# Performance work log

Hardware: AMD Instinct MI355X
Metric: run time of the kernel (lower is better)

Reference implementation:

```python
import jax, jax.numpy as jnp
import numpy as np
from math import sqrt

BASE = 10000.0  # rope_theta
NUM_HEADS = 16


def _quant(x):
    # per-row (last-dim) symmetric int8 fake-quant, matching ActivationQuantSTE.forward
    scale = 127.0 / jnp.maximum(jnp.max(jnp.abs(x), axis=-1, keepdims=True), 1e-5)
    return jnp.clip(jnp.round(x * scale), -128.0, 127.0) / scale


@jax.custom_vjp
def act_quant(x):
    return _quant(x)

def _aq_fwd(x):
    return _quant(x), None

def _aq_bwd(_, g):
    return (g,)  # straight-through estimator

act_quant.defvjp(_aq_fwd, _aq_bwd)


def complex_linear(xr, xi, Wr, Wi):
    # ComplexLinearBase: quantize activations, then
    #   y_real = q_real @ Wr^T + q_imag @ Wi^T
    #   y_imag = q_real @ Wi^T - q_imag @ Wr^T
    qr = act_quant(xr)
    qi = act_quant(xi)
    yr = qr @ Wr.T + qi @ Wi.T
    yi = qr @ Wi.T - qi @ Wr.T
    return yr, yi


def setup_inputs() -> dict:
    T, H = 2048, 2048
    key = jax.random.key(0)
    ks = jax.random.split(key, 10)
    w = lambda k: jax.random.normal(k, (H, H), jnp.float32) * 0.02
    return {
        "hidden_real": jax.random.normal(ks[0], (T, H), jnp.float32),
        "hidden_imag": jax.random.normal(ks[1], (T, H), jnp.float32),
        "positions": jnp.arange(T, dtype=jnp.int32),
        "Wq_r": w(ks[2]), "Wq_i": w(ks[3]),
        "Wk_r": w(ks[4]), "Wk_i": w(ks[5]),
        "Wv_r": w(ks[6]), "Wv_i": w(ks[7]),
        "Wo_r": w(ks[8]), "Wo_i": w(ks[9]),
    }


def reference(hidden_real, hidden_imag, positions, Wq_r, Wq_i, Wk_r, Wk_i, Wv_r, Wv_i, Wo_r, Wo_i):
    T, H = hidden_real.shape
    NH = NUM_HEADS
    D = H // NH  # head_dim

    # complex QKV projections with int8 activation fake-quant
    qr, qi = complex_linear(hidden_real, hidden_imag, Wq_r, Wq_i)
    kr, ki = complex_linear(hidden_real, hidden_imag, Wk_r, Wk_i)
    vr, vi = complex_linear(hidden_real, hidden_imag, Wv_r, Wv_i)

    # Complex RoPE: interleaving (real, imag) then GPT-J-style rotation with
    # head_size = rotary_dim = 2*D is equivalent to rotating (real, imag) pairs:
    #   out_real = real*cos - imag*sin ; out_imag = imag*cos + real*sin
    # inv_freq = base^-(arange(0, 2D, 2)/(2D)) = base^-(arange(D)/D), len D.
    inv_freq = 1.0 / (BASE ** (jnp.arange(D, dtype=jnp.float32) / D))
    freqs = positions.astype(jnp.float32)[:, None] * inv_freq[None, :]  # [T, D]
    # cache is stored in bf16 in the original module
    cos = jnp.cos(freqs).astype(jnp.bfloat16).astype(jnp.float32)[:, None, :]  # [T,1,D]
    sin = jnp.sin(freqs).astype(jnp.bfloat16).astype(jnp.float32)[:, None, :]

    def rope(xr_, xi_):
        r = xr_.reshape(T, NH, D)
        i = xi_.reshape(T, NH, D)
        return r * cos - i * sin, i * cos + r * sin

    qr3, qi3 = rope(qr, qi)
    kr3, ki3 = rope(kr, ki)
    vr3 = vr.reshape(T, NH, D)
    vi3 = vi.reshape(T, NH, D)

    # causal attention; scores = Re(q . conj(k)) / sqrt(2*D)  (complex dim is 2*D)
    scale = 1.0 / sqrt(2 * D)
    scores = (jnp.einsum('thd,shd->hts', qr3, kr3)
              + jnp.einsum('thd,shd->hts', qi3, ki3)) * scale  # [NH, T, T]
    causal = jnp.tril(jnp.ones((T, T), dtype=bool))
    scores = jnp.where(causal[None], scores, -1e9)
    p = jax.nn.softmax(scores, axis=-1)

    out_r = jnp.einsum('hts,shd->thd', p, vr3).reshape(T, H)
    out_i = jnp.einsum('hts,shd->thd', p, vi3).reshape(T, H)

    # complex output projection (with activation fake-quant)
    return complex_linear(out_r, out_i, Wo_r, Wo_i)
```

## Files before the change

### kernel.cpp

```cpp
#include <hip/hip_runtime.h>


typedef float v4f __attribute__((ext_vector_type(4)));
typedef _Float16 v8h __attribute__((ext_vector_type(8)));
typedef _Float16 v4h __attribute__((ext_vector_type(4)));

typedef const __attribute__((address_space(1))) void glob_void;
typedef __attribute__((address_space(3))) void lds_void;

__device__ __forceinline__ void gload16(const _Float16* gp, _Float16* lp) {
  __builtin_amdgcn_global_load_lds((glob_void*)gp, (lds_void*)lp, 16, 0, 0);
}

__device__ __forceinline__ float bf16_rt(float f) {
  union { float f; unsigned u; } a; a.f = f;
  unsigned r = (a.u + 0x7fffu + ((a.u >> 16) & 1u)) & 0xffff0000u;
  union { unsigned u; float f; } b; b.u = r;
  return b.f;
}

#define EPI_QKV 0
#define EPI_OUT 1

__global__ __launch_bounds__(512, 2) void gemm_qkv256(
    const _Float16* __restrict__ A, const _Float16* __restrict__ B,
    _Float16* __restrict__ Yq, _Float16* __restrict__ vt)
{
  const int p = blockIdx.x;
  const int xcd = p & 7, s = p >> 3;
  const int mt = s & 7, ntl = s >> 3;
  const int nt = xcd * 8 + ntl;
  const int m0 = mt << 8;
  const int n0 = nt * 192;

  __shared__ __align__(16) _Float16 lds[57344];

  const int tid = threadIdx.x, lane = tid & 63, wave = tid >> 6;
  const int quad = lane >> 4, l15 = lane & 15;
  const int wm = wave >> 2, wn = wave & 3;

  const int rr = tid >> 2;
  const int lc8 = (((tid & 3) ^ ((tid >> 3) & 3)) << 3);
  const _Float16* gA = A + (long long)(m0 + rr) * 4096 + lc8;
  const _Float16* gBj[3];
#pragma unroll
  for (int j = 0; j < 3; ++j) {
    const int ks = (j == 2) || (j == 1 && tid >= 256);
    const int r = j * 128 + (tid >> 2) - ks * 192;
    gBj[j] = B + (long long)(n0 + r) * 4096 + ks * 32 + lc8;
  }

  const int co = ((quad ^ ((l15 >> 1) & 3)) << 3);
  const int aBase = (wm * 128 + l15) * 32 + co;
  const int bBase = (wn * 48 + l15) * 32 + co;

  v4f acc[8][3] = {};

  auto stage = [&](int b, int k0) {
    _Float16* dst = lds + b * 28672 + tid * 8;
#pragma unroll
    for (int j = 0; j < 4; ++j)
      gload16(gA + k0 + (j & 1) * (128 * 4096) + ((j >> 1) << 5), dst + j * 4096);
#pragma unroll
    for (int j = 0; j < 3; ++j)
      gload16(gBj[j] + k0, dst + 16384 + j * 4096);
  };

  stage(0, 0);

  for (int t = 0; t < 64; ++t) {
    const int buf = t & 1;
    __builtin_amdgcn_s_barrier();
    if (t < 63) {
      stage(buf ^ 1, (t + 1) << 6);
      asm volatile("s_waitcnt vmcnt(7)" ::: "memory");
    } else {
      asm volatile("s_waitcnt vmcnt(0)" ::: "memory");
    }
    __builtin_amdgcn_s_barrier();

    const _Float16* As = lds + buf * 28672;
    const _Float16* Bs = As + 16384;
    v8h bf[3][2];
#pragma unroll
    for (int nf = 0; nf < 3; ++nf)
#pragma unroll
      for (int ks = 0; ks < 2; ++ks)
        bf[nf][ks] = *(const v8h*)&Bs[bBase + ks * 6144 + nf * 512];
#pragma unroll
    for (int mh = 0; mh < 2; ++mh) {
      v8h af[4][2];
#pragma unroll
      for (int i = 0; i < 4; ++i)
#pragma unroll
        for (int ks = 0; ks < 2; ++ks)
          af[i][ks] = *(const v8h*)&As[aBase + ks * 8192 + (mh * 4 + i) * 512];
      __builtin_amdgcn_s_setprio(1);
#pragma unroll
      for (int i = 0; i < 4; ++i)
#pragma unroll
        for (int nf = 0; nf < 3; ++nf)
#pragma unroll
          for (int ks = 0; ks < 2; ++ks)
            acc[mh * 4 + i][nf] = __builtin_amdgcn_mfma_f32_16x16x32_f16(
                af[i][ks], bf[nf][ks], acc[mh * 4 + i][nf], 0, 0, 0);
      __builtin_amdgcn_s_setprio(0);
    }
  }

#pragma unroll
  for (int mf = 0; mf < 8; ++mf) {
#pragma unroll
    for (int nf = 0; nf < 3; ++nf) {
      const int col = n0 + wn * 48 + nf * 16 + l15;
      const int row0 = m0 + wm * 128 + mf * 16 + quad * 4;
      if (col >= 8192) {
        const int c = col - 8192;
        const int hh = (c & 2047) >> 7;
        const int dcol = (c < 2048) ? (c & 127) : (128 + (c & 127));
        v4h pk;
#pragma unroll
        for (int r = 0; r < 4; ++r) pk[r] = (_Float16)acc[mf][nf][r];
        *(v4h*)(vt + ((long long)(hh * 256 + dcol)) * 2048 + row0) = pk;
      } else {
#pragma unroll
        for (int r = 0; r < 4; ++r)
          Yq[(long long)(row0 + r) * 8192 + col] = (_Float16)acc[mf][nf][r];
      }
    }
  }
}

template<int EPI>
__global__ __launch_bounds__(256) void gemm_nt(
    const _Float16* __restrict__ A, const _Float16* __restrict__ B,
    void* __restrict__ Cv, int K, int lda, int ldb, int ldc,
    _Float16* __restrict__ vtout)
{
  const int m0 = blockIdx.x * 128, n0 = blockIdx.y * 128;

  __shared__ __align__(16) _Float16 As[128 * 32];
  __shared__ __align__(16) _Float16 Bs[128 * 32];

  const int tid = threadIdx.x, lane = tid & 63, wave = tid >> 6;
  const int off0 = tid * 8, off1 = 2048 + tid * 8;
  const int r0 = off0 >> 5, r1 = off1 >> 5;
  const int c0 = ((((off0 >> 3) & 3) ^ ((r0 >> 1) & 3)) << 3);
  const int c1 = ((((off1 >> 3) & 3) ^ ((r1 >> 1) & 3)) << 3);
  const _Float16* ga0 = A + (long long)(m0 + r0) * lda + c0;
  const _Float16* ga1 = A + (long long)(m0 + r1) * lda + c1;
  const _Float16* gb0 = B + (long long)(n0 + r0) * ldb + c0;
  const _Float16* gb1 = B + (long long)(n0 + r1) * ldb + c1;

  const int mr = (wave >> 1) * 64 + (lane & 15);
  const int nr = (wave & 1) * 64 + (lane & 15);
  const int kq = lane >> 4;

  v4f acc[4][4] = {};

  for (int k0 = 0; k0 < K; k0 += 32) {
    gload16(ga0 + k0, As + off0);
    gload16(ga1 + k0, As + off1);
    gload16(gb0 + k0, Bs + off0);
    gload16(gb1 + k0, Bs + off1);
    __syncthreads();
    v8h a[4], b[4];
#pragma unroll
    for (int i = 0; i < 4; ++i) {
      const int r = mr + i * 16;
      a[i] = *(const v8h*)&As[r * 32 + ((kq ^ ((r >> 1) & 3)) << 3)];
    }
#pragma unroll
    for (int j = 0; j < 4; ++j) {
      const int r = nr + j * 16;
      b[j] = *(const v8h*)&Bs[r * 32 + ((kq ^ ((r >> 1) & 3)) << 3)];
    }
#pragma unroll
    for (int i = 0; i < 4; ++i)
#pragma unroll
      for (int j = 0; j < 4; ++j)
        acc[i][j] = __builtin_amdgcn_mfma_f32_16x16x32_f16(a[i], b[j], acc[i][j], 0, 0, 0);
    __syncthreads();
  }

  const int cr = (wave >> 1) * 64 + (lane >> 4) * 4;
  const int cc = (wave & 1) * 64 + (lane & 15);
#pragma unroll
  for (int i = 0; i < 4; ++i)
#pragma unroll
    for (int j = 0; j < 4; ++j) {
      const int col = n0 + cc + j * 16;
      if (EPI == EPI_QKV && col >= 8192) {
        const int c = col - 8192;
        const int hh = (c & 2047) >> 7;
        const int dcol = (c < 2048) ? (c & 127) : (128 + (c & 127));
        const int row0 = m0 + cr + i * 16;
        v4h pk;
#pragma unroll
        for (int r = 0; r < 4; ++r) pk[r] = (_Float16)acc[i][j][r];
        *(v4h*)(vtout + ((long long)(hh * 256 + dcol)) * 2048 + row0) = pk;
      } else {
#pragma unroll
        for (int r = 0; r < 4; ++r) {
          const int row = m0 + cr + i * 16 + r;
          const float v = acc[i][j][r];
          if (EPI == EPI_QKV) {
            ((_Float16*)Cv)[(long long)row * ldc + col] = (_Float16)v;
          } else {
            float* O = (float*)Cv;
            if (col < 2048) O[(long long)row * 2048 + col] = v;
            else O[2048ll * 2048 + (long long)row * 2048 + (col - 2048)] = v;
          }
        }
      }
    }
}

__global__ __launch_bounds__(256) void quant_rows(
    const float* __restrict__ s0, const float* __restrict__ s1,
    _Float16* __restrict__ dst)
{
  const int t = blockIdx.x, y = blockIdx.y;
  const float* src = (y ? s1 : s0) + (long long)t * 2048;
  const int tid = threadIdx.x, lane = tid & 63, wave = tid >> 6;
  __shared__ float rbuf[4];
  const v4f a = *(const v4f*)(src + tid * 4);
  const v4f b = *(const v4f*)(src + 1024 + tid * 4);
  float m = 0.f;
#pragma unroll
  for (int k = 0; k < 4; ++k)
    m = fmaxf(m, fmaxf(fabsf(a[k]), fabsf(b[k])));
  for (int o = 1; o < 64; o <<= 1) m = fmaxf(m, __shfl_xor(m, o, 64));
  if (lane == 0) rbuf[wave] = m;
  __syncthreads();
  m = fmaxf(fmaxf(rbuf[0], rbuf[1]), fmaxf(rbuf[2], rbuf[3]));
  const float scale = 127.f / fmaxf(m, 1e-5f);
  const float inv = 1.f / scale;
  _Float16* d = dst + (long long)t * 4096 + (long long)y * 2048 + tid * 4;
  v4h qa, qb;
#pragma unroll
  for (int k = 0; k < 4; ++k) {
    qa[k] = (_Float16)(fminf(fmaxf(rintf(a[k] * scale), -128.f), 127.f) * inv);
    qb[k] = (_Float16)(fminf(fmaxf(rintf(b[k] * scale), -128.f), 127.f) * inv);
  }
  *(v4h*)d = qa;
  *(v4h*)(d + 1024) = qb;
}

__global__ __launch_bounds__(256) void wprep(
    const float* __restrict__ Wq_r, const float* __restrict__ Wq_i,
    const float* __restrict__ Wk_r, const float* __restrict__ Wk_i,
    const float* __restrict__ Wv_r, const float* __restrict__ Wv_i,
    const float* __restrict__ Wo_r, const float* __restrict__ Wo_i,
    _Float16* __restrict__ Bqkv, _Float16* __restrict__ Bo)
{
  const float* Ws[8] = {Wq_r, Wq_i, Wk_r, Wk_i, Wv_r, Wv_i, Wo_r, Wo_i};
  const int i = blockIdx.x * 256 + threadIdx.x;
  const int w = i >> 18;
  const int rem = i & 262143;
  const int j = rem >> 7;
  const int cb = (rem & 127) * 16;
  const float* src = Ws[w] + (long long)j * 2048 + cb;
  _Float16* Bp = (w < 6) ? (Bqkv + (long long)(w >> 1) * 4096 * 4096) : Bo;
  const int isI = w & 1;
  _Float16* d1 = Bp + (long long)j * 4096 + (isI ? 2048 + cb : cb);
  _Float16* d2 = Bp + (long long)(2048 + j) * 4096 + (isI ? cb : 2048 + cb);
  const float sg2 = isI ? 1.f : -1.f;
#pragma unroll
  for (int q = 0; q < 4; ++q) {
    const v4f v = *(const v4f*)(src + q * 4);
    v4h o1, o2;
#pragma unroll
    for (int k = 0; k < 4; ++k) {
      o1[k] = (_Float16)v[k];
      o2[k] = (_Float16)(v[k] * sg2);
    }
    *(v4h*)(d1 + q * 4) = o1;
    *(v4h*)(d2 + q * 4) = o2;
  }
}

__global__ __launch_bounds__(256) void trig_kernel(
    const int* __restrict__ pos, float* __restrict__ cs)
{
  const int t = blockIdx.x * 2 + (threadIdx.x >> 7);
  const int d = threadIdx.x & 127;
  const float invf = (float)pow(10000.0, -(double)d / 128.0);
  const float fr = (float)pos[t] * invf;
  const double fd = (double)fr;
  cs[((long long)t * 128 + d) * 2]     = bf16_rt((float)cos(fd));
  cs[((long long)t * 128 + d) * 2 + 1] = bf16_rt((float)sin(fd));
}

__global__ __launch_bounds__(256) void rope_kernel(
    const _Float16* __restrict__ Yq, const float* __restrict__ cs,
    _Float16* __restrict__ qc, _Float16* __restrict__ kc)
{
  const int idx = blockIdx.x * 256 + threadIdx.x;
  const int d0 = (idx & 15) * 8;
  const int h  = (idx >> 4) & 15;
  const int t  = idx >> 8;
  const _Float16* y = Yq + (long long)t * 8192 + h * 128 + d0;
  const v8h qr8 = *(const v8h*)(y);
  const v8h qi8 = *(const v8h*)(y + 2048);
  const v8h kr8 = *(const v8h*)(y + 4096);
  const v8h ki8 = *(const v8h*)(y + 6144);
  const float* cp = cs + ((long long)t * 128 + d0) * 2;
  v8h qro, qio, kro, kio;
#pragma unroll
  for (int u = 0; u < 8; ++u) {
    const float c = cp[u * 2], s = cp[u * 2 + 1];
    const float qr = (float)qr8[u], qi = (float)qi8[u];
    const float kr = (float)kr8[u], ki = (float)ki8[u];
    qro[u] = (_Float16)(qr * c - qi * s);
    qio[u] = (_Float16)(qi * c + qr * s);
    kro[u] = (_Float16)(kr * c - ki * s);
    kio[u] = (_Float16)(ki * c + kr * s);
  }
  _Float16* qo = qc + ((long long)h * 2048 + t) * 256 + d0;
  _Float16* ko = kc + ((long long)h * 2048 + t) * 256 + d0;
  *(v8h*)qo = qro; *(v8h*)(qo + 128) = qio;
  *(v8h*)ko = kro; *(v8h*)(ko + 128) = kio;
}

__global__ __launch_bounds__(256, 2) void flash_attn(
    const _Float16* __restrict__ qc, const _Float16* __restrict__ kc,
    const _Float16* __restrict__ vt, float* __restrict__ attn)
{
  __shared__ __align__(16) _Float16 Ps[64 * 72];
  __shared__ float pmax[2][64];
  __shared__ float psum[2][64];

  const int h  = blockIdx.y;
  const int qt = ((h >> 3) & 1) ? (31 - (int)blockIdx.x) : (int)blockIdx.x;
  const int q0 = qt * 64;
  const int tid = threadIdx.x, lane = tid & 63, wave = tid >> 6;
  const int mi = wave >> 1, ni = wave & 1;
  const int quad = lane >> 4, l15 = lane & 15;

  const _Float16* qh = qc + (long long)h * 2048 * 256;
  const _Float16* kh = kc + (long long)h * 2048 * 256;
  const _Float16* vh = vt + (long long)h * 256 * 2048;

  const _Float16 scl = (_Float16)0.09016844f;
  v8h qf[2][8];
#pragma unroll
  for (int mt = 0; mt < 2; ++mt) {
    const int t = q0 + mi * 32 + mt * 16 + l15;
#pragma unroll
    for (int ks = 0; ks < 8; ++ks) {
      v8h q = *(const v8h*)(qh + (long long)t * 256 + ks * 32 + quad * 8);
#pragma unroll
      for (int u = 0; u < 8; ++u) q[u] *= scl;
      qf[mt][ks] = q;
    }
  }

  float mrow[2][4], lrow[2][4];
  v4f acc_o[2][8];
#pragma unroll
  for (int mt = 0; mt < 2; ++mt)
#pragma unroll
    for (int r = 0; r < 4; ++r) { mrow[mt][r] = -1e30f; lrow[mt][r] = 0.f; }
#pragma unroll
  for (int mt = 0; mt < 2; ++mt)
#pragma unroll
    for (int nt = 0; nt < 8; ++nt) acc_o[mt][nt] = (v4f){0.f, 0.f, 0.f, 0.f};

  for (int st = 0; st <= qt; ++st) {
    const int s0 = st * 64;

    v4f sa[2][2] = {};
#pragma unroll
    for (int ks = 0; ks < 8; ++ks) {
      v8h bk[2];
#pragma unroll
      for (int jn = 0; jn < 2; ++jn)
        bk[jn] = *(const v8h*)(kh + (long long)(s0 + ni * 32 + jn * 16 + l15) * 256
                               + ks * 32 + quad * 8);
#pragma unroll
      for (int mt = 0; mt < 2; ++mt)
#pragma unroll
        for (int jn = 0; jn < 2; ++jn)
          sa[mt][jn] = __builtin_amdgcn_mfma_f32_16x16x32_f16(qf[mt][ks], bk[jn], sa[mt][jn], 0, 0, 0);
    }

    const bool diag = (st == qt);
    float pm[2][4];
#pragma unroll
    for (int mt = 0; mt < 2; ++mt)
#pragma unroll
      for (int r = 0; r < 4; ++r) pm[mt][r] = -1e30f;
#pragma unroll
    for (int mt = 0; mt < 2; ++mt)
#pragma unroll
      for (int jn = 0; jn < 2; ++jn)
#pragma unroll
        for (int r = 0; r < 4; ++r) {
          float v = sa[mt][jn][r];
          if (diag) {
            const int rl = mi * 32 + mt * 16 + quad * 4 + r;
            const int cl = ni * 32 + jn * 16 + l15;
            if (cl > rl) v = -1e30f;
          }
          sa[mt][jn][r] = v;
          pm[mt][r] = fmaxf(pm[mt][r], v);
        }
#pragma unroll
    for (int o = 1; o < 16; o <<= 1)
#pragma unroll
      for (int mt = 0; mt < 2; ++mt)
#pragma unroll
        for (int r = 0; r < 4; ++r)
          pm[mt][r] = fmaxf(pm[mt][r], __shfl_xor(pm[mt][r], o, 64));
    if (l15 == 0) {
#pragma unroll
      for (int mt = 0; mt < 2; ++mt)
#pragma unroll
        for (int r = 0; r < 4; ++r)
          pmax[ni][mi * 32 + mt * 16 + quad * 4 + r] = pm[mt][r];
    }
    __syncthreads();

    float al[2][4], ps[2][4];
#pragma unroll
    for (int mt = 0; mt < 2; ++mt)
#pragma unroll
      for (int r = 0; r < 4; ++r) {
        const int row = mi * 32 + mt * 16 + quad * 4 + r;
        const float mn = fmaxf(mrow[mt][r], fmaxf(pmax[0][row], pmax[1][row]));
        al[mt][r] = __builtin_amdgcn_exp2f(mrow[mt][r] - mn);
        mrow[mt][r] = mn;
        ps[mt][r] = 0.f;
      }
#pragma unroll
    for (int mt = 0; mt < 2; ++mt)
#pragma unroll
      for (int jn = 0; jn < 2; ++jn)
#pragma unroll
        for (int r = 0; r < 4; ++r) {
          const float e = __builtin_amdgcn_exp2f(sa[mt][jn][r] - mrow[mt][r]);
          ps[mt][r] += e;
          Ps[(mi * 32 + mt * 16 + quad * 4 + r) * 72 + ni * 32 + jn * 16 + l15] = (_Float16)e;
        }
#pragma unroll
    for (int o = 1; o < 16; o <<= 1)
#pragma unroll
      for (int mt = 0; mt < 2; ++mt)
#pragma unroll
        for (int r = 0; r < 4; ++r)
          ps[mt][r] += __shfl_xor(ps[mt][r], o, 64);
    if (l15 == 0) {
#pragma unroll
      for (int mt = 0; mt < 2; ++mt)
#pragma unroll
        for (int r = 0; r < 4; ++r)
          psum[ni][mi * 32 + mt * 16 + quad * 4 + r] = ps[mt][r];
    }
    __syncthreads();

#pragma unroll
    for (int mt = 0; mt < 2; ++mt)
#pragma unroll
      for (int r = 0; r < 4; ++r) {
        const int row = mi * 32 + mt * 16 + quad * 4 + r;
        lrow[mt][r] = lrow[mt][r] * al[mt][r] + psum[0][row] + psum[1][row];
      }
#pragma unroll
    for (int mt = 0; mt < 2; ++mt)
#pragma unroll
      for (int nt = 0; nt < 8; ++nt)
#pragma unroll
        for (int r = 0; r < 4; ++r)
          acc_o[mt][nt][r] *= al[mt][r];

#pragma unroll
    for (int kc2 = 0; kc2 < 2; ++kc2) {
      v8h pa[2];
#pragma unroll
      for (int mt = 0; mt < 2; ++mt) {
        const int row = mi * 32 + mt * 16 + l15;
        pa[mt] = *(const v8h*)(Ps + row * 72 + kc2 * 32 + quad * 8);
      }
#pragma unroll
      for (int nt = 0; nt < 8; ++nt) {
        const v8h vb = *(const v8h*)(vh + (long long)(ni * 128 + nt * 16 + l15) * 2048
                                     + s0 + kc2 * 32 + quad * 8);
#pragma unroll
        for (int mt = 0; mt < 2; ++mt)
          acc_o[mt][nt] = __builtin_amdgcn_mfma_f32_16x16x32_f16(pa[mt], vb, acc_o[mt][nt], 0, 0, 0);
      }
    }
  }

#pragma unroll
  for (int mt = 0; mt < 2; ++mt) {
    float inv[4];
#pragma unroll
    for (int r = 0; r < 4; ++r) inv[r] = 1.f / lrow[mt][r];
#pragma unroll
    for (int nt = 0; nt < 8; ++nt) {
      const int d = ni * 128 + nt * 16 + l15;
      float* dst = attn + ((d < 128) ? 0ll : (2048ll * 2048)) + (h * 128 + (d & 127));
#pragma unroll
      for (int r = 0; r < 4; ++r) {
        const int t = q0 + mi * 32 + mt * 16 + quad * 4 + r;
        dst[(long long)t * 2048] = acc_o[mt][nt][r] * inv[r];
      }
    }
  }
}

extern "C" void kernel_launch(void* const* d_in, const int* in_sizes, int n_in,
                              void* d_out, int out_size, void* d_ws, size_t ws_size,
                              hipStream_t stream) {
  const float* hr   = (const float*)d_in[0];
  const float* hi   = (const float*)d_in[1];
  const int*   pos  = (const int*)d_in[2];
  const float* Wq_r = (const float*)d_in[3];
  const float* Wq_i = (const float*)d_in[4];
  const float* Wk_r = (const float*)d_in[5];
  const float* Wk_i = (const float*)d_in[6];
  const float* Wv_r = (const float*)d_in[7];
  const float* Wv_i = (const float*)d_in[8];
  const float* Wo_r = (const float*)d_in[9];
  const float* Wo_i = (const float*)d_in[10];

  char* ws = (char*)d_ws;
  _Float16* Bqkv = (_Float16*)(ws);
  float*    attn = (float*)   (ws);
  float*    cs   = (float*)   (ws + (32ll  << 20));
  _Float16* Bo   = (_Float16*)(ws + (96ll  << 20));
  _Float16* Ac   = (_Float16*)(ws + (128ll << 20));
  _Float16* Yq   = (_Float16*)(ws + (144ll << 20));
  _Float16* qc   = (_Float16*)(ws + (176ll << 20));
  _Float16* kc   = (_Float16*)(ws + (192ll << 20));
  _Float16* vt   = (_Float16*)(ws + (208ll << 20));

  quant_rows<<<dim3(2048, 2), 256, 0, stream>>>(hr, hi, Ac);
  wprep<<<8192, 256, 0, stream>>>(Wq_r, Wq_i, Wk_r, Wk_i, Wv_r, Wv_i, Wo_r, Wo_i, Bqkv, Bo);
  gemm_qkv256<<<512, 512, 0, stream>>>(Ac, Bqkv, Yq, vt);
  trig_kernel<<<1024, 256, 0, stream>>>(pos, cs);
  rope_kernel<<<2048, 256, 0, stream>>>(Yq, cs, qc, kc);
  flash_attn<<<dim3(32, 16), 256, 0, stream>>>(qc, kc, vt, attn);
  quant_rows<<<dim3(2048, 2), 256, 0, stream>>>(attn, attn + 2048ll * 2048, Ac);
  gemm_nt<EPI_OUT><<<dim3(16, 32), 256, 0, stream>>>(
      Ac, Bo, d_out, 4096, 4096, 4096, 0, nullptr);
}
```

Before: 735.0 us.

## Interleave QKV GEMM global-to-LDS staging with MFMA phases in ping-pong schedule

Restructures the QKV projection GEMM main loop into four sub-phases per k-tile. Each phase issues a slice of the next tile's global-to-LDS loads alongside LDS fragment reads and a 12-MFMA cluster, with explicit barriers and vmcnt waits, instead of staging the whole tile up front. This spreads memory traffic across the compute and reduces fragment register pressure. It adds several workgroup barriers per iteration, and the split vmcnt bookkeeping is fragile.

```diff
diff --git a/kernel.cpp b/kernel.cpp
--- a/kernel.cpp
+++ b/kernel.cpp
@@ -21,6 +21,10 @@
 
 #define EPI_QKV 0
 #define EPI_OUT 1
+
+#define SBAR()  __builtin_amdgcn_sched_barrier(0)
+#define WBAR()  __builtin_amdgcn_s_barrier()
+#define LGKM0() asm volatile("s_waitcnt lgkmcnt(0)" ::: "memory")
 
 __global__ __launch_bounds__(512, 2) void gemm_qkv256(
     const _Float16* __restrict__ A, const _Float16* __restrict__ B,
@@ -56,56 +60,96 @@
 
   v4f acc[8][3] = {};
 
-  auto stage = [&](int b, int k0) {
-    _Float16* dst = lds + b * 28672 + tid * 8;
-#pragma unroll
-    for (int j = 0; j < 4; ++j)
-      gload16(gA + k0 + (j & 1) * (128 * 4096) + ((j >> 1) << 5), dst + j * 4096);
-#pragma unroll
-    for (int j = 0; j < 3; ++j)
-      gload16(gBj[j] + k0, dst + 16384 + j * 4096);
-  };
-
-  stage(0, 0);
+  {
+    _Float16* sd = lds + tid * 8;
+    gload16(gA, sd);
+    gload16(gA + 524288, sd + 4096);
+    gload16(gBj[0], sd + 16384);
+    gload16(gBj[1], sd + 20480);
+    gload16(gA + 32, sd + 8192);
+    gload16(gA + 524288 + 32, sd + 12288);
+    gload16(gBj[2], sd + 24576);
+  }
+  asm volatile("s_waitcnt vmcnt(3)" ::: "memory");
+  WBAR();
 
   for (int t = 0; t < 64; ++t) {
-    const int buf = t & 1;
-    __builtin_amdgcn_s_barrier();
-    if (t < 63) {
-      stage(buf ^ 1, (t + 1) << 6);
-      asm volatile("s_waitcnt vmcnt(7)" ::: "memory");
-    } else {
-      asm volatile("s_waitcnt vmcnt(0)" ::: "memory");
-    }
-    __builtin_amdgcn_s_barrier();
-
-    const _Float16* As = lds + buf * 28672;
+    const _Float16* As = lds + (t & 1) * 28672;
     const _Float16* Bs = As + 16384;
-    v8h bf[3][2];
-#pragma unroll
-    for (int nf = 0; nf < 3; ++nf)
-#pragma unroll
-      for (int ks = 0; ks < 2; ++ks)
-        bf[nf][ks] = *(const v8h*)&Bs[bBase + ks * 6144 + nf * 512];
-#pragma unroll
-    for (int mh = 0; mh < 2; ++mh) {
-      v8h af[4][2];
-#pragma unroll
-      for (int i = 0; i < 4; ++i)
-#pragma unroll
-        for (int ks = 0; ks < 2; ++ks)
-          af[i][ks] = *(const v8h*)&As[aBase + ks * 8192 + (mh * 4 + i) * 512];
-      __builtin_amdgcn_s_setprio(1);
-#pragma unroll
-      for (int i = 0; i < 4; ++i)
-#pragma unroll
-        for (int nf = 0; nf < 3; ++nf)
-#pragma unroll
-          for (int ks = 0; ks < 2; ++ks)
-            acc[mh * 4 + i][nf] = __builtin_amdgcn_mfma_f32_16x16x32_f16(
-                af[i][ks], bf[nf][ks], acc[mh * 4 + i][nf], 0, 0, 0);
-      __builtin_amdgcn_s_setprio(0);
-    }
+    _Float16* sd = lds + ((t & 1) ^ 1) * 28672 + tid * 8;
+    const int k1 = (t + 1) << 6;
+    const bool stg = (t < 63);
+
+    v8h bf[3], af[4];
+
+    af[0] = *(const v8h*)&As[aBase];
+    af[1] = *(const v8h*)&As[aBase + 512];
+    af[2] = *(const v8h*)&As[aBase + 1024];
+    af[3] = *(const v8h*)&As[aBase + 1536];
+    bf[0] = *(const v8h*)&Bs[bBase];
+    bf[1] = *(const v8h*)&Bs[bBase + 512];
+    bf[2] = *(const v8h*)&Bs[bBase + 1024];
+    if (stg) { gload16(gA + k1, sd); gload16(gA + k1 + 524288, sd + 4096); }
+    SBAR(); WBAR(); LGKM0(); SBAR();
+    __builtin_amdgcn_s_setprio(1);
+#pragma unroll
+    for (int i = 0; i < 4; ++i)
+#pragma unroll
+      for (int nf = 0; nf < 3; ++nf)
+        acc[i][nf] = __builtin_amdgcn_mfma_f32_16x16x32_f16(af[i], bf[nf], acc[i][nf], 0, 0, 0);
+    __builtin_amdgcn_s_setprio(0);
+    WBAR();
+
+    af[0] = *(const v8h*)&As[aBase + 2048];
+    af[1] = *(const v8h*)&As[aBase + 2560];
+    af[2] = *(const v8h*)&As[aBase + 3072];
+    af[3] = *(const v8h*)&As[aBase + 3584];
+    if (stg) { gload16(gBj[0] + k1, sd + 16384); gload16(gBj[1] + k1, sd + 20480); }
+    SBAR(); WBAR(); LGKM0(); SBAR();
+    __builtin_amdgcn_s_setprio(1);
+#pragma unroll
+    for (int i = 0; i < 4; ++i)
+#pragma unroll
+      for (int nf = 0; nf < 3; ++nf)
+        acc[4 + i][nf] = __builtin_amdgcn_mfma_f32_16x16x32_f16(af[i], bf[nf], acc[4 + i][nf], 0, 0, 0);
+    __builtin_amdgcn_s_setprio(0);
+    if (stg) asm volatile("s_waitcnt vmcnt(4)" ::: "memory");
+    else     asm volatile("s_waitcnt vmcnt(0)" ::: "memory");
+    WBAR();
+
+    bf[0] = *(const v8h*)&Bs[bBase + 6144];
+    bf[1] = *(const v8h*)&Bs[bBase + 6656];
+    bf[2] = *(const v8h*)&Bs[bBase + 7168];
+    af[0] = *(const v8h*)&As[aBase + 8192];
+    af[1] = *(const v8h*)&As[aBase + 8704];
+    af[2] = *(const v8h*)&As[aBase + 9216];
+    af[3] = *(const v8h*)&As[aBase + 9728];
+    if (stg) { gload16(gA + k1 + 32, sd + 8192); gload16(gA + k1 + 524288 + 32, sd + 12288); }
+    SBAR(); WBAR(); LGKM0(); SBAR();
+    __builtin_amdgcn_s_setprio(1);
+#pragma unroll
+    for (int i = 0; i < 4; ++i)
+#pragma unroll
+      for (int nf = 0; nf < 3; ++nf)
+        acc[i][nf] = __builtin_amdgcn_mfma_f32_16x16x32_f16(af[i], bf[nf], acc[i][nf], 0, 0, 0);
+    __builtin_amdgcn_s_setprio(0);
+    WBAR();
+
+    af[0] = *(const v8h*)&As[aBase + 10240];
+    af[1] = *(const v8h*)&As[aBase + 10752];
+    af[2] = *(const v8h*)&As[aBase + 11264];
+    af[3] = *(const v8h*)&As[aBase + 11776];
+    if (stg) gload16(gBj[2] + k1, sd + 24576);
+    SBAR(); WBAR(); LGKM0(); SBAR();
+    __builtin_amdgcn_s_setprio(1);
+#pragma unroll
+    for (int i = 0; i < 4; ++i)
+#pragma unroll
+      for (int nf = 0; nf < 3; ++nf)
+        acc[4 + i][nf] = __builtin_amdgcn_mfma_f32_16x16x32_f16(af[i], bf[nf], acc[4 + i][nf], 0, 0, 0);
+    __builtin_amdgcn_s_setprio(0);
+    if (stg) asm volatile("s_waitcnt vmcnt(3)" ::: "memory");
+    WBAR();
   }
 
 #pragma unroll
```

Result: no change. 729.9 us (-0.7%).
